# Kernel optimization log

Measured on AMD Instinct MI355X. Metric: run time of the kernel, lower is better.

Reference implementation:

```python
import jax, jax.numpy as jnp
import numpy as np

NUM_EDGE_TYPES = 8
HIDDEN = 128
N_NODES = 50000
N_EDGES = 600000


def setup_inputs() -> dict:
    key = jax.random.key(0)
    ks = jax.random.split(key, 10)
    H = HIDDEN
    h = jax.random.normal(ks[0], (N_NODES, H), dtype=jnp.float32)
    edge_index = jax.random.randint(ks[1], (2, N_EDGES), 0, N_NODES, dtype=jnp.int32)
    edge_type = jax.random.randint(ks[2], (N_EDGES,), 0, NUM_EDGE_TYPES + 1, dtype=jnp.int32)
    s = 1.0 / np.sqrt(H)
    W_msg = jax.random.uniform(ks[3], (H, H), jnp.float32, -s, s)
    b_msg = jax.random.uniform(ks[4], (H,), jnp.float32, -s, s)
    edge_embed = jax.random.normal(ks[5], (NUM_EDGE_TYPES + 1, H), dtype=jnp.float32)
    W_ih = jax.random.uniform(ks[6], (3 * H, H), jnp.float32, -s, s)
    W_hh = jax.random.uniform(ks[7], (3 * H, H), jnp.float32, -s, s)
    b_ih = jax.random.uniform(ks[8], (3 * H,), jnp.float32, -s, s)
    b_hh = jax.random.uniform(ks[9], (3 * H,), jnp.float32, -s, s)
    return {"h": h, "edge_index": edge_index, "edge_type": edge_type,
            "num_nodes": N_NODES, "W_msg": W_msg, "b_msg": b_msg,
            "edge_embed": edge_embed, "W_ih": W_ih, "W_hh": W_hh,
            "b_ih": b_ih, "b_hh": b_hh}


def _gru_cell(x, h, W_ih, W_hh, b_ih, b_hh):
    # PyTorch GRUCell: gates ordered (r, z, n)
    H = h.shape[-1]
    gi = x @ W_ih.T + b_ih  # (N, 3H)
    gh = h @ W_hh.T + b_hh
    i_r, i_z, i_n = gi[:, :H], gi[:, H:2 * H], gi[:, 2 * H:]
    h_r, h_z, h_n = gh[:, :H], gh[:, H:2 * H], gh[:, 2 * H:]
    r = jax.nn.sigmoid(i_r + h_r)
    z = jax.nn.sigmoid(i_z + h_z)
    n = jnp.tanh(i_n + r * h_n)
    return (1.0 - z) * n + z * h


def reference(h, edge_index, edge_type, num_nodes, W_msg, b_msg, edge_embed, W_ih, W_hh, b_ih, b_hh):
    src = edge_index[0]
    dst = edge_index[1]
    # gather -> linear -> edge-type embed add
    src_h = h[src] @ W_msg.T + b_msg                      # (E, H)
    emb = edge_embed[jnp.clip(edge_type, 0, NUM_EDGE_TYPES)]  # (E, H)
    msg = src_h + emb
    # scatter-add into per-node message buffer
    messages = jax.ops.segment_sum(msg, dst, num_segments=num_nodes)  # (num_nodes, H)
    h_new = _gru_cell(messages, h[:num_nodes], W_ih, W_hh, b_ih, b_hh)
    result = jnp.zeros_like(h).at[:num_nodes].set(h_new)
    return result
```

## Files before the change

kernel.cpp:

```cpp
#include <hip/hip_runtime.h>
#include <math.h>

#define H 128
typedef unsigned int u32;
typedef unsigned long long u64;
typedef __attribute__((ext_vector_type(8))) short short8;
typedef __attribute__((ext_vector_type(4))) float floatx4;

#define XS_STRIDE 136
#define CS_STRIDE 40
#define ROWCAP 48

__device__ __forceinline__ float sigmoid_f(float x) {
    return 1.0f / (1.0f + __expf(-x));
}
__device__ __forceinline__ float tanh_f(float x) {
    float t = __expf(-2.0f * fabsf(x));
    float r = (1.0f - t) / (1.0f + t);
    return copysignf(r, x);
}
__device__ __forceinline__ unsigned short f2bf(float x) {
    u32 u = __float_as_uint(x);
    return (unsigned short)((u + 0x7fffu + ((u >> 16) & 1u)) >> 16);
}
__device__ __forceinline__ float bf2f(unsigned short s) {
    return __uint_as_float(((u32)s) << 16);
}
__device__ __forceinline__ float bf_lo32(u32 u) { return __uint_as_float(u << 16); }
__device__ __forceinline__ float bf_hi32(u32 u) { return __uint_as_float(u & 0xffff0000u); }

__global__ __launch_bounds__(256) void fused_pre_kernel(
    const float* __restrict__ h, unsigned short* __restrict__ h_b, int total8,
    int* __restrict__ head4, int N,
    const float* __restrict__ Wih, const float* __restrict__ Whh,
    const float* __restrict__ Wm,  const float* __restrict__ emb,
    const float* __restrict__ bm,
    unsigned short* __restrict__ Wcs, unsigned short* __restrict__ Whhs,
    unsigned short* __restrict__ embWs, int HB, int DB)
{
    int b = blockIdx.x;
    if (b < HB) {
        int idx = b * 256 + threadIdx.x;
        if (idx >= total8) return;
        const float4* p = (const float4*)(h + (size_t)idx * 8);
        float4 a = p[0], bb = p[1];
        short8 v;
        v[0] = (short)f2bf(a.x);  v[1] = (short)f2bf(a.y);
        v[2] = (short)f2bf(a.z);  v[3] = (short)f2bf(a.w);
        v[4] = (short)f2bf(bb.x); v[5] = (short)f2bf(bb.y);
        v[6] = (short)f2bf(bb.z); v[7] = (short)f2bf(bb.w);
        *(short8*)(h_b + (size_t)idx * 8) = v;
        return;
    }
    if (b < HB + DB) {
        int idx = (b - HB) * 256 + threadIdx.x;
        if (idx < 4 * N) head4[idx] = -1;
        return;
    }
    int idx = (b - HB - DB) * 256 + threadIdx.x;
    if (idx < 49152) {
        int g = idx >> 7;
        int k = idx & 127;
        float acc = 0.f;
#pragma unroll 4
        for (int c = 0; c < H; ++c)
            acc += Wih[(size_t)g * H + c] * Wm[(size_t)c * H + k];
        int gate = g >> 7;
        int wi = g & 127;
        int j = wi >> 4, m = wi & 15;
        int kc = k >> 5, q = (k >> 3) & 3, i = k & 7;
        int l = q * 16 + m;
        Wcs[(size_t)(((gate * 8 + j) * 4 + kc) * 64 + l) * 8 + i] = f2bf(acc);
    } else if (idx < 61440) {
        int s = idx - 49152;
        int i = s & 7;
        int l = (s >> 3) & 63;
        int jb = s >> 9;
        int gate = jb >> 3, jj = jb & 7;
        int q = l >> 4, m = l & 15;
        int t = q * 8 + i;
        unsigned short v = 0;
        if (t < 9) {
            int g = gate * 128 + jj * 16 + m;
            float acc = 0.f;
#pragma unroll 4
            for (int jx = 0; jx < H; ++jx)
                acc += (emb[(size_t)t * H + jx] + bm[jx]) * Wih[(size_t)g * H + jx];
            v = f2bf(acc);
        }
        embWs[s] = v;
    } else if (idx < 67584) {
        int t2 = idx - 61440;
        int l  = t2 & 63;
        int kc = (t2 >> 6) & 3;
        int jr = t2 >> 8;
        int m = l & 15, q = l >> 4;
        size_t srco = (size_t)(jr * 16 + m) * H + kc * 32 + q * 8;
        const float4* s0 = (const float4*)(Whh + srco);
        float4 a = s0[0], bb = s0[1];
        short8 v;
        v[0] = (short)f2bf(a.x);  v[1] = (short)f2bf(a.y);
        v[2] = (short)f2bf(a.z);  v[3] = (short)f2bf(a.w);
        v[4] = (short)f2bf(bb.x); v[5] = (short)f2bf(bb.y);
        v[6] = (short)f2bf(bb.z); v[7] = (short)f2bf(bb.w);
        *(short8*)(Whhs + (size_t)t2 * 8) = v;
    }
}

__global__ __launch_bounds__(256) void fill_ll_kernel(
    const int* __restrict__ eidx, const int* __restrict__ etype,
    int* __restrict__ head4, int* __restrict__ nexte,
    int* __restrict__ packed, int E)
{
    int e = blockIdx.x * 256 + threadIdx.x;
    if (e >= E) return;
    int src = eidx[e];
    int dst = eidx[E + e];
    int t = etype[e];
    t = t < 0 ? 0 : (t > 8 ? 8 : t);
    packed[e] = src | (t << 24);
    int old = atomicExch(&head4[(size_t)dst * 4 + (e & 3)], e);
    nexte[e] = old;
}

__global__ __launch_bounds__(256) void gather_fused_kernel(
    const unsigned short* __restrict__ h_b,
    const int* __restrict__ head4, int* __restrict__ nexte,
    const int* __restrict__ packed,
    unsigned short* __restrict__ S_b, u64* __restrict__ cnt, int N)
{
    __shared__ int rowbuf[64 * ROWCAP];
    __shared__ int lcnt[64];
    __shared__ int lohead[64];

    int tid = threadIdx.x;
    if (tid < 64) { lcnt[tid] = 0; lohead[tid] = -1; }
    __syncthreads();

    {
        int k = tid >> 2;
        int cch = tid & 3;
        int n = blockIdx.x * 64 + k;
        if (n < N) {
            int e = head4[(size_t)n * 4 + cch];
            while (e >= 0) {
                int nx = nexte[e];
                int u = packed[e];
                int p = atomicAdd(&lcnt[k], 1);
                if (p < ROWCAP) {
                    rowbuf[k * ROWCAP + p] = u;
                } else {
                    nexte[e] = atomicExch(&lohead[k], e);
                }
                e = nx;
            }
        }
    }
    __syncthreads();

    int lane = tid & 63;
    int wv = tid >> 6;
    for (int t = 0; t < 16; ++t) {
        int kk = wv * 16 + t;
        int n = blockIdx.x * 64 + kk;
        if (n >= N) break;
        int m = lcnt[kk];
        m = m < ROWCAP ? m : ROWCAP;
        const int* row = &rowbuf[kk * ROWCAP];

        float ax = 0.f, ay = 0.f;
        u64 c = 0;
        int i = 0;
        for (; i + 8 <= m; i += 8) {
            int u0 = row[i + 0];
            int u1 = row[i + 1];
            int u2 = row[i + 2];
            int u3 = row[i + 3];
            int u4 = row[i + 4];
            int u5 = row[i + 5];
            int u6 = row[i + 6];
            int u7 = row[i + 7];
            u32 x0 = *((const u32*)(h_b + (size_t)(u0 & 0xffffff) * H) + lane);
            u32 x1 = *((const u32*)(h_b + (size_t)(u1 & 0xffffff) * H) + lane);
            u32 x2 = *((const u32*)(h_b + (size_t)(u2 & 0xffffff) * H) + lane);
            u32 x3 = *((const u32*)(h_b + (size_t)(u3 & 0xffffff) * H) + lane);
            u32 x4 = *((const u32*)(h_b + (size_t)(u4 & 0xffffff) * H) + lane);
            u32 x5 = *((const u32*)(h_b + (size_t)(u5 & 0xffffff) * H) + lane);
            u32 x6 = *((const u32*)(h_b + (size_t)(u6 & 0xffffff) * H) + lane);
            u32 x7 = *((const u32*)(h_b + (size_t)(u7 & 0xffffff) * H) + lane);
            c += (1ull << (7 * (u0 >> 24))) + (1ull << (7 * (u1 >> 24)))
               + (1ull << (7 * (u2 >> 24))) + (1ull << (7 * (u3 >> 24)))
               + (1ull << (7 * (u4 >> 24))) + (1ull << (7 * (u5 >> 24)))
               + (1ull << (7 * (u6 >> 24))) + (1ull << (7 * (u7 >> 24)));
            ax += bf_lo32(x0) + bf_lo32(x1) + bf_lo32(x2) + bf_lo32(x3)
                + bf_lo32(x4) + bf_lo32(x5) + bf_lo32(x6) + bf_lo32(x7);
            ay += bf_hi32(x0) + bf_hi32(x1) + bf_hi32(x2) + bf_hi32(x3)
                + bf_hi32(x4) + bf_hi32(x5) + bf_hi32(x6) + bf_hi32(x7);
        }
        for (; i + 4 <= m; i += 4) {
            int u0 = row[i + 0];
            int u1 = row[i + 1];
            int u2 = row[i + 2];
            int u3 = row[i + 3];
            u32 x0 = *((const u32*)(h_b + (size_t)(u0 & 0xffffff) * H) + lane);
            u32 x1 = *((const u32*)(h_b + (size_t)(u1 & 0xffffff) * H) + lane);
            u32 x2 = *((const u32*)(h_b + (size_t)(u2 & 0xffffff) * H) + lane);
            u32 x3 = *((const u32*)(h_b + (size_t)(u3 & 0xffffff) * H) + lane);
            c += (1ull << (7 * (u0 >> 24))) + (1ull << (7 * (u1 >> 24)))
               + (1ull << (7 * (u2 >> 24))) + (1ull << (7 * (u3 >> 24)));
            ax += bf_lo32(x0) + bf_lo32(x1) + bf_lo32(x2) + bf_lo32(x3);
            ay += bf_hi32(x0) + bf_hi32(x1) + bf_hi32(x2) + bf_hi32(x3);
        }
        for (; i < m; ++i) {
            int u = row[i];
            u32 x = *((const u32*)(h_b + (size_t)(u & 0xffffff) * H) + lane);
            c += 1ull << (7 * (u >> 24));
            ax += bf_lo32(x);
            ay += bf_hi32(x);
        }
        int oh = lohead[kk];
        if (oh >= 0) {
            int ecur = oh;
            while (ecur >= 0) {
                int u = packed[ecur];
                u32 x = *((const u32*)(h_b + (size_t)(u & 0xffffff) * H) + lane);
                c += 1ull << (7 * (u >> 24));
                ax += bf_lo32(x);
                ay += bf_hi32(x);
                ecur = nexte[ecur];
            }
        }
        u32 o = (u32)f2bf(ax) | ((u32)f2bf(ay) << 16);
        *((u32*)(S_b + (size_t)n * H) + lane) = o;
        if (lane == 0) cnt[n] = c;
    }
}

__global__ __launch_bounds__(256, 4) void gru_mfma_kernel(
    const unsigned short* __restrict__ S_b, const unsigned short* __restrict__ h_b,
    const unsigned short* __restrict__ Wcs, const unsigned short* __restrict__ Whhs,
    const unsigned short* __restrict__ embWs,
    const float* __restrict__ bih, const float* __restrict__ bhh,
    const u64* __restrict__ cnt,
    const int* __restrict__ numn, float* __restrict__ out, int N)
{
    __shared__ unsigned short xs[64 * XS_STRIDE];
    __shared__ unsigned short hsb[64 * XS_STRIDE];
    __shared__ unsigned short cs[64 * CS_STRIDE];

    int tid = threadIdx.x;
    int bx = blockIdx.x;
    int node0 = (bx >> 1) * 64;
    int jhalf = bx & 1;

    int lane = tid & 63;
    int wv = tid >> 6;
    int j = jhalf * 4 + wv;

    short8 er = *(const short8*)(embWs + (size_t)((0 * 8 + j) * 64 + lane) * 8);
    short8 ez = *(const short8*)(embWs + (size_t)((1 * 8 + j) * 64 + lane) * 8);
    short8 en = *(const short8*)(embWs + (size_t)((2 * 8 + j) * 64 + lane) * 8);

    for (int c = tid; c < 1024; c += 256) {
        int r = c >> 4;
        int k8 = (c & 15) << 3;
        int n = node0 + r;
        int nc = n < N ? n : N - 1;
        *(short8*)(&xs[r * XS_STRIDE + k8]) =
            *(const short8*)(S_b + (size_t)nc * H + k8);
        *(short8*)(&hsb[r * XS_STRIDE + k8]) =
            *(const short8*)(h_b + (size_t)nc * H + k8);
    }
    {
        int r = tid >> 2, tg = tid & 3;
        int n = node0 + r;
        u64 cv = cnt[n < N ? n : N - 1];
        short8 v = {0, 0, 0, 0, 0, 0, 0, 0};
        if (tg == 0) {
#pragma unroll
            for (int i = 0; i < 8; ++i)
                v[i] = (short)f2bf((float)((u32)(cv >> (7 * i)) & 127u));
        } else if (tg == 1) {
            v[0] = (short)f2bf((float)((u32)(cv >> 56) & 127u));
        }
        *(short8*)(&cs[r * CS_STRIDE + tg * 8]) = v;
    }
    __syncthreads();

    int am = lane & 15;
    int aq = lane >> 4;

    int num_nodes = numn[0];
    floatx4 zero = {0.f, 0.f, 0.f, 0.f};

    floatx4 aR[4], aZ[4], aIn[4], aHn[4];
#pragma unroll
    for (int rt = 0; rt < 4; ++rt) {
        short8 acn = *(const short8*)(&cs[(rt * 16 + am) * CS_STRIDE + aq * 8]);
        aR[rt]  = __builtin_amdgcn_mfma_f32_16x16x32_bf16(acn, er, zero, 0, 0, 0);
        aZ[rt]  = __builtin_amdgcn_mfma_f32_16x16x32_bf16(acn, ez, zero, 0, 0, 0);
        aIn[rt] = __builtin_amdgcn_mfma_f32_16x16x32_bf16(acn, en, zero, 0, 0, 0);
        aHn[rt] = zero;
    }
#pragma unroll
    for (int kc = 0; kc < 4; ++kc) {
        size_t c_r = (size_t)(((0 * 8 + j) * 4 + kc) * 64 + lane) * 8;
        size_t c_z = (size_t)(((1 * 8 + j) * 4 + kc) * 64 + lane) * 8;
        size_t c_n = (size_t)(((2 * 8 + j) * 4 + kc) * 64 + lane) * 8;
        short8 bir = *(const short8*)(Wcs + c_r);
        short8 bhr = *(const short8*)(Whhs + c_r);
        short8 biz = *(const short8*)(Wcs + c_z);
        short8 bhz = *(const short8*)(Whhs + c_z);
        short8 bin = *(const short8*)(Wcs + c_n);
        short8 bhn = *(const short8*)(Whhs + c_n);
#pragma unroll
        for (int rt = 0; rt < 4; ++rt) {
            int arow = rt * 16 + am;
            short8 axv = *(const short8*)(&xs[arow * XS_STRIDE + kc * 32 + aq * 8]);
            short8 ahv = *(const short8*)(&hsb[arow * XS_STRIDE + kc * 32 + aq * 8]);
            aR[rt]  = __builtin_amdgcn_mfma_f32_16x16x32_bf16(axv, bir, aR[rt], 0, 0, 0);
            aR[rt]  = __builtin_amdgcn_mfma_f32_16x16x32_bf16(ahv, bhr, aR[rt], 0, 0, 0);
            aZ[rt]  = __builtin_amdgcn_mfma_f32_16x16x32_bf16(axv, biz, aZ[rt], 0, 0, 0);
            aZ[rt]  = __builtin_amdgcn_mfma_f32_16x16x32_bf16(ahv, bhz, aZ[rt], 0, 0, 0);
            aIn[rt] = __builtin_amdgcn_mfma_f32_16x16x32_bf16(axv, bin, aIn[rt], 0, 0, 0);
            aHn[rt] = __builtin_amdgcn_mfma_f32_16x16x32_bf16(ahv, bhn, aHn[rt], 0, 0, 0);
        }
    }
    int c = j * 16 + am;
    float b_r = bih[c]       + bhh[c];
    float b_z = bih[128 + c] + bhh[128 + c];
    float b_in = bih[256 + c], b_hn = bhh[256 + c];
#pragma unroll
    for (int rt = 0; rt < 4; ++rt) {
#pragma unroll
        for (int q = 0; q < 4; ++q) {
            int m = rt * 16 + aq * 4 + q;
            int node = node0 + m;
            if (node < N) {
                float r  = sigmoid_f(aR[rt][q] + b_r);
                float z  = sigmoid_f(aZ[rt][q] + b_z);
                float nv = tanh_f((aIn[rt][q] + b_in) + r * (aHn[rt][q] + b_hn));
                float hv = bf2f(hsb[m * XS_STRIDE + c]);
                float o  = (1.0f - z) * nv + z * hv;
                out[(size_t)node * H + c] = (node < num_nodes) ? o : 0.0f;
            }
        }
    }
}

extern "C" void kernel_launch(void* const* d_in, const int* in_sizes, int n_in,
                              void* d_out, int out_size, void* d_ws, size_t ws_size,
                              hipStream_t stream) {
    const float* h    = (const float*)d_in[0];
    const int*  eidx  = (const int*)d_in[1];
    const int*  etype = (const int*)d_in[2];
    const int*  numn  = (const int*)d_in[3];
    const float* Wm   = (const float*)d_in[4];
    const float* bm   = (const float*)d_in[5];
    const float* emb  = (const float*)d_in[6];
    const float* Wih  = (const float*)d_in[7];
    const float* Whh  = (const float*)d_in[8];
    const float* bih  = (const float*)d_in[9];
    const float* bhh  = (const float*)d_in[10];

    int N = in_sizes[0] / H;
    int E = in_sizes[2];

    unsigned short* S_b   = (unsigned short*)d_ws;
    unsigned short* h_b   = S_b + (size_t)N * H;
    unsigned short* Wcs   = h_b + (size_t)N * H;
    unsigned short* Whhs  = Wcs + 3 * H * H;
    unsigned short* embWs = Whhs + 3 * H * H;
    u64* cnt    = (u64*)(embWs + 12288);
    int* head4  = (int*)(cnt + N);
    int* packed = head4 + 4 * N;
    int* nexte  = packed + E;

    int total8 = N * H / 8;
    int HB = (total8 + 255) / 256;
    int DB = (4 * N + 255) / 256;
    int PB = 264;
    fused_pre_kernel<<<HB + DB + PB, 256, 0, stream>>>(
        h, h_b, total8, head4, N, Wih, Whh, Wm, emb, bm,
        Wcs, Whhs, embWs, HB, DB);

    fill_ll_kernel<<<(E + 255) / 256, 256, 0, stream>>>(
        eidx, etype, head4, nexte, packed, E);

    gather_fused_kernel<<<(N + 63) / 64, 256, 0, stream>>>(
        h_b, head4, nexte, packed, S_b, cnt, N);

    int nblk = ((N + 63) / 64) * 2;
    gru_mfma_kernel<<<nblk, 256, 0, stream>>>(S_b, h_b, Wcs, Whhs, embWs,
                                              bih, bhh, cnt, numn, (float*)d_out, N);
}
```

Before: 202.5 us.

## Fuse neighbor gather and GRU MFMA into one 512-thread kernel

Merges the gather/aggregate kernel and the GRU MFMA kernel into a single kernel with 512 threads per 64-node block. Aggregated messages and edge-type counts now go straight to shared memory instead of through a global S_b/cnt round trip. The upper 256 threads load the h tile while the lower ones build the edge lists. Each block now computes all 8 output column groups with 8 waves, rather than two blocks per node tile doing half each. The cost is higher shared memory and register use per block, which may lower occupancy, and the gather now has 8 waves instead of 4 to spread its latency over.

New measurement: 198.8 us. No clear change (-1.8%).

```diff
diff --git a/kernel.cpp b/kernel.cpp
--- a/kernel.cpp
+++ b/kernel.cpp
@@ -123,24 +123,39 @@
     nexte[e] = old;
 }
 
-__global__ __launch_bounds__(256) void gather_fused_kernel(
+__global__ __launch_bounds__(512, 4) void gather_gru_kernel(
     const unsigned short* __restrict__ h_b,
     const int* __restrict__ head4, int* __restrict__ nexte,
     const int* __restrict__ packed,
-    unsigned short* __restrict__ S_b, u64* __restrict__ cnt, int N)
+    const unsigned short* __restrict__ Wcs, const unsigned short* __restrict__ Whhs,
+    const unsigned short* __restrict__ embWs,
+    const float* __restrict__ bih, const float* __restrict__ bhh,
+    const int* __restrict__ numn, float* __restrict__ out, int N)
 {
+    __shared__ unsigned short xs[64 * XS_STRIDE];
+    __shared__ unsigned short hsb[64 * XS_STRIDE];
+    __shared__ unsigned short cs[64 * CS_STRIDE];
     __shared__ int rowbuf[64 * ROWCAP];
     __shared__ int lcnt[64];
     __shared__ int lohead[64];
 
     int tid = threadIdx.x;
+    int node0 = blockIdx.x * 64;
+    int lane = tid & 63;
+    int wv = tid >> 6;
+    int j = wv;
+
+    short8 er = *(const short8*)(embWs + (size_t)((0 * 8 + j) * 64 + lane) * 8);
+    short8 ez = *(const short8*)(embWs + (size_t)((1 * 8 + j) * 64 + lane) * 8);
+    short8 en = *(const short8*)(embWs + (size_t)((2 * 8 + j) * 64 + lane) * 8);
+
     if (tid < 64) { lcnt[tid] = 0; lohead[tid] = -1; }
     __syncthreads();
 
-    {
+    if (tid < 256) {
         int k = tid >> 2;
         int cch = tid & 3;
-        int n = blockIdx.x * 64 + k;
+        int n = node0 + k;
         if (n < N) {
             int e = head4[(size_t)n * 4 + cch];
             while (e >= 0) {
@@ -155,141 +170,103 @@
                 e = nx;
             }
         }
+    } else {
+        int idx = tid - 256;
+#pragma unroll
+        for (int q = 0; q < 4; ++q) {
+            int c = idx * 4 + q;
+            int r = c >> 4;
+            int k8 = (c & 15) << 3;
+            int n = node0 + r;
+            int nc = n < N ? n : N - 1;
+            *(short8*)(&hsb[r * XS_STRIDE + k8]) =
+                *(const short8*)(h_b + (size_t)nc * H + k8);
+        }
     }
     __syncthreads();
 
-    int lane = tid & 63;
-    int wv = tid >> 6;
-    for (int t = 0; t < 16; ++t) {
-        int kk = wv * 16 + t;
-        int n = blockIdx.x * 64 + kk;
-        if (n >= N) break;
-        int m = lcnt[kk];
-        m = m < ROWCAP ? m : ROWCAP;
-        const int* row = &rowbuf[kk * ROWCAP];
-
-        float ax = 0.f, ay = 0.f;
-        u64 c = 0;
-        int i = 0;
-        for (; i + 8 <= m; i += 8) {
-            int u0 = row[i + 0];
-            int u1 = row[i + 1];
-            int u2 = row[i + 2];
-            int u3 = row[i + 3];
-            int u4 = row[i + 4];
-            int u5 = row[i + 5];
-            int u6 = row[i + 6];
-            int u7 = row[i + 7];
-            u32 x0 = *((const u32*)(h_b + (size_t)(u0 & 0xffffff) * H) + lane);
-            u32 x1 = *((const u32*)(h_b + (size_t)(u1 & 0xffffff) * H) + lane);
-            u32 x2 = *((const u32*)(h_b + (size_t)(u2 & 0xffffff) * H) + lane);
-            u32 x3 = *((const u32*)(h_b + (size_t)(u3 & 0xffffff) * H) + lane);
-            u32 x4 = *((const u32*)(h_b + (size_t)(u4 & 0xffffff) * H) + lane);
-            u32 x5 = *((const u32*)(h_b + (size_t)(u5 & 0xffffff) * H) + lane);
-            u32 x6 = *((const u32*)(h_b + (size_t)(u6 & 0xffffff) * H) + lane);
-            u32 x7 = *((const u32*)(h_b + (size_t)(u7 & 0xffffff) * H) + lane);
-            c += (1ull << (7 * (u0 >> 24))) + (1ull << (7 * (u1 >> 24)))
-               + (1ull << (7 * (u2 >> 24))) + (1ull << (7 * (u3 >> 24)))
-               + (1ull << (7 * (u4 >> 24))) + (1ull << (7 * (u5 >> 24)))
-               + (1ull << (7 * (u6 >> 24))) + (1ull << (7 * (u7 >> 24)));
-            ax += bf_lo32(x0) + bf_lo32(x1) + bf_lo32(x2) + bf_lo32(x3)
-                + bf_lo32(x4) + bf_lo32(x5) + bf_lo32(x6) + bf_lo32(x7);
-            ay += bf_hi32(x0) + bf_hi32(x1) + bf_hi32(x2) + bf_hi32(x3)
-                + bf_hi32(x4) + bf_hi32(x5) + bf_hi32(x6) + bf_hi32(x7);
-        }
-        for (; i + 4 <= m; i += 4) {
-            int u0 = row[i + 0];
-            int u1 = row[i + 1];
-            int u2 = row[i + 2];
-            int u3 = row[i + 3];
-            u32 x0 = *((const u32*)(h_b + (size_t)(u0 & 0xffffff) * H) + lane);
-            u32 x1 = *((const u32*)(h_b + (size_t)(u1 & 0xffffff) * H) + lane);
-            u32 x2 = *((const u32*)(h_b + (size_t)(u2 & 0xffffff) * H) + lane);
-            u32 x3 = *((const u32*)(h_b + (size_t)(u3 & 0xffffff) * H) + lane);
-            c += (1ull << (7 * (u0 >> 24))) + (1ull << (7 * (u1 >> 24)))
-               + (1ull << (7 * (u2 >> 24))) + (1ull << (7 * (u3 >> 24)));
-            ax += bf_lo32(x0) + bf_lo32(x1) + bf_lo32(x2) + bf_lo32(x3);
-            ay += bf_hi32(x0) + bf_hi32(x1) + bf_hi32(x2) + bf_hi32(x3);
-        }
-        for (; i < m; ++i) {
-            int u = row[i];
-            u32 x = *((const u32*)(h_b + (size_t)(u & 0xffffff) * H) + lane);
-            c += 1ull << (7 * (u >> 24));
-            ax += bf_lo32(x);
-            ay += bf_hi32(x);
-        }
-        int oh = lohead[kk];
-        if (oh >= 0) {
-            int ecur = oh;
-            while (ecur >= 0) {
-                int u = packed[ecur];
+    for (int tt = 0; tt < 8; ++tt) {
+        int kk = wv * 8 + tt;
+        int n = node0 + kk;
+        if (n < N) {
+            int m = lcnt[kk];
+            m = m < ROWCAP ? m : ROWCAP;
+            const int* row = &rowbuf[kk * ROWCAP];
+
+            float ax = 0.f, ay = 0.f;
+            u64 c = 0;
+            int i = 0;
+            for (; i + 8 <= m; i += 8) {
+                int u0 = row[i + 0];
+                int u1 = row[i + 1];
+                int u2 = row[i + 2];
+                int u3 = row[i + 3];
+                int u4 = row[i + 4];
+                int u5 = row[i + 5];
+                int u6 = row[i + 6];
+                int u7 = row[i + 7];
+                u32 x0 = *((const u32*)(h_b + (size_t)(u0 & 0xffffff) * H) + lane);
+                u32 x1 = *((const u32*)(h_b + (size_t)(u1 & 0xffffff) * H) + lane);
+                u32 x2 = *((const u32*)(h_b + (size_t)(u2 & 0xffffff) * H) + lane);
+                u32 x3 = *((const u32*)(h_b + (size_t)(u3 & 0xffffff) * H) + lane);
+                u32 x4 = *((const u32*)(h_b + (size_t)(u4 & 0xffffff) * H) + lane);
+                u32 x5 = *((const u32*)(h_b + (size_t)(u5 & 0xffffff) * H) + lane);
+                u32 x6 = *((const u32*)(h_b + (size_t)(u6 & 0xffffff) * H) + lane);
+                u32 x7 = *((const u32*)(h_b + (size_t)(u7 & 0xffffff) * H) + lane);
+                c += (1ull << (7 * (u0 >> 24))) + (1ull << (7 * (u1 >> 24)))
+                   + (1ull << (7 * (u2 >> 24))) + (1ull << (7 * (u3 >> 24)))
+                   + (1ull << (7 * (u4 >> 24))) + (1ull << (7 * (u5 >> 24)))
+                   + (1ull << (7 * (u6 >> 24))) + (1ull << (7 * (u7 >> 24)));
+                ax += bf_lo32(x0) + bf_lo32(x1) + bf_lo32(x2) + bf_lo32(x3)
+                    + bf_lo32(x4) + bf_lo32(x5) + bf_lo32(x6) + bf_lo32(x7);
+                ay += bf_hi32(x0) + bf_hi32(x1) + bf_hi32(x2) + bf_hi32(x3)
+                    + bf_hi32(x4) + bf_hi32(x5) + bf_hi32(x6) + bf_hi32(x7);
+            }
+            for (; i + 4 <= m; i += 4) {
+                int u0 = row[i + 0];
+                int u1 = row[i + 1];
+                int u2 = row[i + 2];
+                int u3 = row[i + 3];
+                u32 x0 = *((const u32*)(h_b + (size_t)(u0 & 0xffffff) * H) + lane);
+                u32 x1 = *((const u32*)(h_b + (size_t)(u1 & 0xffffff) * H) + lane);
+                u32 x2 = *((const u32*)(h_b + (size_t)(u2 & 0xffffff) * H) + lane);
+                u32 x3 = *((const u32*)(h_b + (size_t)(u3 & 0xffffff) * H) + lane);
+                c += (1ull << (7 * (u0 >> 24))) + (1ull << (7 * (u1 >> 24)))
+                   + (1ull << (7 * (u2 >> 24))) + (1ull << (7 * (u3 >> 24)));
+                ax += bf_lo32(x0) + bf_lo32(x1) + bf_lo32(x2) + bf_lo32(x3);
+                ay += bf_hi32(x0) + bf_hi32(x1) + bf_hi32(x2) + bf_hi32(x3);
+            }
+            for (; i < m; ++i) {
+                int u = row[i];
                 u32 x = *((const u32*)(h_b + (size_t)(u & 0xffffff) * H) + lane);
                 c += 1ull << (7 * (u >> 24));
                 ax += bf_lo32(x);
                 ay += bf_hi32(x);
-                ecur = nexte[ecur];
-            }
-        }
-        u32 o = (u32)f2bf(ax) | ((u32)f2bf(ay) << 16);
-        *((u32*)(S_b + (size_t)n * H) + lane) = o;
-        if (lane == 0) cnt[n] = c;
-    }
-}
-
-__global__ __launch_bounds__(256, 4) void gru_mfma_kernel(
-    const unsigned short* __restrict__ S_b, const unsigned short* __restrict__ h_b,
-    const unsigned short* __restrict__ Wcs, const unsigned short* __restrict__ Whhs,
-    const unsigned short* __restrict__ embWs,
-    const float* __restrict__ bih, const float* __restrict__ bhh,
-    const u64* __restrict__ cnt,
-    const int* __restrict__ numn, float* __restrict__ out, int N)
-{
-    __shared__ unsigned short xs[64 * XS_STRIDE];
-    __shared__ unsigned short hsb[64 * XS_STRIDE];
-    __shared__ unsigned short cs[64 * CS_STRIDE];
-
-    int tid = threadIdx.x;
-    int bx = blockIdx.x;
-    int node0 = (bx >> 1) * 64;
-    int jhalf = bx & 1;
-
-    int lane = tid & 63;
-    int wv = tid >> 6;
-    int j = jhalf * 4 + wv;
-
-    short8 er = *(const short8*)(embWs + (size_t)((0 * 8 + j) * 64 + lane) * 8);
-    short8 ez = *(const short8*)(embWs + (size_t)((1 * 8 + j) * 64 + lane) * 8);
-    short8 en = *(const short8*)(embWs + (size_t)((2 * 8 + j) * 64 + lane) * 8);
-
-    for (int c = tid; c < 1024; c += 256) {
-        int r = c >> 4;
-        int k8 = (c & 15) << 3;
-        int n = node0 + r;
-        int nc = n < N ? n : N - 1;
-        *(short8*)(&xs[r * XS_STRIDE + k8]) =
-            *(const short8*)(S_b + (size_t)nc * H + k8);
-        *(short8*)(&hsb[r * XS_STRIDE + k8]) =
-            *(const short8*)(h_b + (size_t)nc * H + k8);
-    }
-    {
-        int r = tid >> 2, tg = tid & 3;
-        int n = node0 + r;
-        u64 cv = cnt[n < N ? n : N - 1];
-        short8 v = {0, 0, 0, 0, 0, 0, 0, 0};
-        if (tg == 0) {
-#pragma unroll
-            for (int i = 0; i < 8; ++i)
-                v[i] = (short)f2bf((float)((u32)(cv >> (7 * i)) & 127u));
-        } else if (tg == 1) {
-            v[0] = (short)f2bf((float)((u32)(cv >> 56) & 127u));
-        }
-        *(short8*)(&cs[r * CS_STRIDE + tg * 8]) = v;
+            }
+            int oh = lohead[kk];
+            if (oh >= 0) {
+                int ecur = oh;
+                while (ecur >= 0) {
+                    int u = packed[ecur];
+                    u32 x = *((const u32*)(h_b + (size_t)(u & 0xffffff) * H) + lane);
+                    c += 1ull << (7 * (u >> 24));
+                    ax += bf_lo32(x);
+                    ay += bf_hi32(x);
+                    ecur = nexte[ecur];
+                }
+            }
+            u32 o = (u32)f2bf(ax) | ((u32)f2bf(ay) << 16);
+            ((u32*)&xs[kk * XS_STRIDE])[lane] = o;
+            if (lane < 32)
+                cs[kk * CS_STRIDE + lane] =
+                    (lane < 9) ? f2bf((float)((u32)(c >> (7 * lane)) & 127u))
+                               : (unsigned short)0;
+        }
     }
     __syncthreads();
 
     int am = lane & 15;
     int aq = lane >> 4;
-
     int num_nodes = numn[0];
     floatx4 zero = {0.f, 0.f, 0.f, 0.f};
 
@@ -366,13 +343,11 @@
     int N = in_sizes[0] / H;
     int E = in_sizes[2];
 
-    unsigned short* S_b   = (unsigned short*)d_ws;
-    unsigned short* h_b   = S_b + (size_t)N * H;
+    unsigned short* h_b   = (unsigned short*)d_ws;
     unsigned short* Wcs   = h_b + (size_t)N * H;
     unsigned short* Whhs  = Wcs + 3 * H * H;
     unsigned short* embWs = Whhs + 3 * H * H;
-    u64* cnt    = (u64*)(embWs + 12288);
-    int* head4  = (int*)(cnt + N);
+    int* head4  = (int*)(embWs + 12288);
     int* packed = head4 + 4 * N;
     int* nexte  = packed + E;
 
@@ -387,10 +362,7 @@
     fill_ll_kernel<<<(E + 255) / 256, 256, 0, stream>>>(
         eidx, etype, head4, nexte, packed, E);
 
-    gather_fused_kernel<<<(N + 63) / 64, 256, 0, stream>>>(
-        h_b, head4, nexte, packed, S_b, cnt, N);
-
-    int nblk = ((N + 63) / 64) * 2;
-    gru_mfma_kernel<<<nblk, 256, 0, stream>>>(S_b, h_b, Wcs, Whhs, embWs,
-                                              bih, bhh, cnt, numn, (float*)d_out, N);
-}
+    gather_gru_kernel<<<(N + 63) / 64, 512, 0, stream>>>(
+        h_b, head4, nexte, packed, Wcs, Whhs, embWs,
+        bih, bhh, numn, (float*)d_out, N);
+}
```
